# Kernel tuning notes

Measured on AMD Instinct MI355X. Metric: run time of the kernel, lower is better.

The kernel has to match this reference:

```python
import jax, jax.numpy as jnp
import numpy as np

N_NODES = 100000
N_EDGES = 3200000


def gcn_conv(x, edge_index, W, b, num_nodes):
    """PyG GCNConv: x' = D^{-1/2} (A + I) D^{-1/2} (x W) + b (symmetric norm, self-loops)."""
    x = x @ W  # [N, out]
    loop = jnp.arange(num_nodes, dtype=edge_index.dtype)
    src = jnp.concatenate([edge_index[0], loop])
    dst = jnp.concatenate([edge_index[1], loop])
    # degree over destination nodes (incl. self loops)
    deg = jax.ops.segment_sum(jnp.ones_like(dst, dtype=x.dtype), dst, num_segments=num_nodes)
    dinv = jnp.where(deg > 0, jax.lax.rsqrt(deg), 0.0)
    norm = dinv[src] * dinv[dst]  # [E + N]
    msg = x[src] * norm[:, None]  # gather + scale
    out = jax.ops.segment_sum(msg, dst, num_segments=num_nodes)  # scatter-add
    return out + b


def setup_inputs() -> dict:
    key = jax.random.key(0)
    k = jax.random.split(key, 5)
    x = jax.random.normal(k[0], (N_NODES, 256), dtype=jnp.float32)
    edge_index = jax.random.randint(k[1], (2, N_EDGES), 0, N_NODES, dtype=jnp.int64)
    W1 = jax.random.normal(k[2], (256, 16), dtype=jnp.float32) * (1.0 / np.sqrt(256))
    b1 = jnp.zeros((16,), dtype=jnp.float32)
    W2 = jax.random.normal(k[3], (16, 8), dtype=jnp.float32) * (1.0 / np.sqrt(16))
    b2 = jnp.zeros((8,), dtype=jnp.float32)
    return {"x": x, "edge_index": edge_index, "W1": W1, "b1": b1, "W2": W2, "b2": b2}


def reference(x, edge_index, W1, b1, W2, b2):
    n = x.shape[0]
    h = gcn_conv(x, edge_index, W1, b1, n)
    h = jax.nn.relu(h)
    # dropout is identity in eval mode (training=False)
    h = gcn_conv(h, edge_index, W2, b2, n)
    return jax.nn.log_softmax(h, axis=1)
```

## Files before the change

### kernel.cpp

```cpp
#include <hip/hip_runtime.h>

#define NN 100000
#define NE 3200000
#define NB 391
#define CAP 9216
#define PB 16
#define CH_A (256 * PB)
#define FXS 65536.0f
#define FXI (1.0f / 65536.0f)

typedef _Float16 half4 __attribute__((ext_vector_type(4)));
typedef _Float16 half8 __attribute__((ext_vector_type(8)));

__device__ __forceinline__ float4 f4fma(float s, float4 a, float4 c) {
  c.x = fmaf(s, a.x, c.x); c.y = fmaf(s, a.y, c.y);
  c.z = fmaf(s, a.z, c.z); c.w = fmaf(s, a.w, c.w);
  return c;
}

template<int CTRL>
__device__ __forceinline__ float4 quad_bcast(float4 v) {
  float4 r;
  r.x = __int_as_float(__builtin_amdgcn_update_dpp(__float_as_int(v.x), __float_as_int(v.x), CTRL, 0xF, 0xF, false));
  r.y = __int_as_float(__builtin_amdgcn_update_dpp(__float_as_int(v.y), __float_as_int(v.y), CTRL, 0xF, 0xF, false));
  r.z = __int_as_float(__builtin_amdgcn_update_dpp(__float_as_int(v.z), __float_as_int(v.z), CTRL, 0xF, 0xF, false));
  r.w = __int_as_float(__builtin_amdgcn_update_dpp(__float_as_int(v.w), __float_as_int(v.w), CTRL, 0xF, 0xF, false));
  return r;
}

__global__ __launch_bounds__(256) void bin_kernel(const int* __restrict__ ei,
                                                  int* __restrict__ bucket_cursor,
                                                  int* __restrict__ pairs) {
  __shared__ int  cnt[4][NB];
  __shared__ int  wcur[4][NB];
  __shared__ int  lbase[NB];
  __shared__ int  gbase[NB];
  __shared__ int  sc[512];
  __shared__ int2 stage[CH_A];
  __shared__ int  w64flag;
  int t = threadIdx.x;
  int wv = t >> 6;
  for (int k = t; k < 4 * NB; k += 256) (&cnt[0][0])[k] = 0;
  if (t < 64) {
    int o = (t < 32) ? ei[2 * t + 1] : 0;
    unsigned long long bl = __ballot(o != 0);
    if (t == 0) w64flag = (bl == 0ULL) ? 1 : 0;
  }
  __syncthreads();
  bool w64 = (w64flag != 0);
  int base = blockIdx.x * CH_A;
  int nval = min(CH_A, NE - base);
  int s[PB], d[PB];
  if (w64) {
#pragma unroll
    for (int i = 0; i < 8; ++i) {
      int e0 = base + i * 512 + 2 * t;
      if (e0 < NE) {
        int4 svv = *(const int4*)(ei + 2 * (size_t)e0);
        int4 dvv = *(const int4*)(ei + 2 * (size_t)NE + 2 * (size_t)e0);
        s[2 * i] = svv.x; s[2 * i + 1] = svv.z;
        d[2 * i] = dvv.x; d[2 * i + 1] = dvv.z;
        atomicAdd(&cnt[wv][dvv.x >> 8], 1);
        atomicAdd(&cnt[wv][dvv.z >> 8], 1);
      } else {
        d[2 * i] = -1; d[2 * i + 1] = -1;
      }
    }
  } else {
#pragma unroll
    for (int i = 0; i < PB; ++i) {
      int e = base + i * 256 + t;
      if (e < NE) {
        s[i] = ei[e];
        d[i] = ei[NE + e];
        atomicAdd(&cnt[wv][d[i] >> 8], 1);
      } else {
        d[i] = -1;
      }
    }
  }
  __syncthreads();
  int tA = (t < NB) ? cnt[0][t] + cnt[1][t] + cnt[2][t] + cnt[3][t] : 0;
  int tB = (t + 256 < NB) ? cnt[0][t + 256] + cnt[1][t + 256] + cnt[2][t + 256] + cnt[3][t + 256] : 0;
  sc[t] = tA; sc[t + 256] = tB;
  __syncthreads();
#pragma unroll
  for (int off = 1; off < 512; off <<= 1) {
    int u0 = (t >= off) ? sc[t - off] : 0;
    int u1 = (t + 256 >= off) ? sc[t + 256 - off] : 0;
    __syncthreads();
    sc[t] += u0; sc[t + 256] += u1;
    __syncthreads();
  }
#pragma unroll
  for (int h = 0; h < 2; ++h) {
    int k = t + h * 256;
    if (k < NB) {
      int tot = (h == 0) ? tA : tB;
      int lb = sc[k] - tot;
      lbase[k] = lb;
      gbase[k] = (tot > 0) ? atomicAdd(&bucket_cursor[k], tot) : 0;
      int c0 = cnt[0][k], c1 = cnt[1][k], c2 = cnt[2][k];
      wcur[0][k] = lb;
      wcur[1][k] = lb + c0;
      wcur[2][k] = lb + c0 + c1;
      wcur[3][k] = lb + c0 + c1 + c2;
    }
  }
  __syncthreads();
#pragma unroll
  for (int i = 0; i < PB; ++i) {
    if (d[i] >= 0) {
      int b = d[i] >> 8;
      int slot = atomicAdd(&wcur[wv][b], 1);
      stage[slot] = make_int2(s[i], d[i]);
    }
  }
  __syncthreads();
  for (int k = t; k < nval; k += 256) {
    int2 p = stage[k];
    int b = p.y >> 8;
    pairs[(size_t)b * CAP + gbase[b] + (k - lbase[b])] = p.x | ((p.y & 255) << 24);
  }
}

__global__ __launch_bounds__(512) void hist_kernel(const int* __restrict__ pairs,
                                                   const int* __restrict__ bucket_cursor,
                                                   float* __restrict__ dinv) {
  __shared__ int hist[2][256];
  int t = threadIdx.x;
  int b = blockIdx.x;
  int cnt_b = bucket_cursor[b];
  size_t in_base = (size_t)b * CAP;
  if (t < 256) { hist[0][t] = 0; hist[1][t] = 0; }
  __syncthreads();
  int hs = t >> 8;
  for (int i = t; i < cnt_b; i += 512) {
    int pk = pairs[in_base + i];
    atomicAdd(&hist[hs][((unsigned)pk) >> 24], 1);
  }
  __syncthreads();
  if (t < 256) {
    int n = b * 256 + t;
    if (n < NN)
      dinv[n] = rsqrtf((float)(hist[0][t] + hist[1][t]) + 1.0f);
  }
}

__global__ __launch_bounds__(256) void gemm1_kernel(const float* __restrict__ x,
                                                    const float* __restrict__ W1,
                                                    const float* __restrict__ dinv,
                                                    _Float16* __restrict__ xw1h) {
  const int lane = threadIdx.x & 63;
  const int wv   = threadIdx.x >> 6;
  const int node0 = (blockIdx.x * 4 + wv) * 8;
  const int cg = lane >> 2;
  const int jl = lane & 3;
  float4 w[16];
#pragma unroll
  for (int k = 0; k < 4; ++k)
#pragma unroll
    for (int c = 0; c < 4; ++c)
      w[k * 4 + c] = *(const float4*)(W1 + (cg * 16 + k * 4 + c) * 16 + jl * 4);
  float4 xv[8];
#pragma unroll
  for (int i = 0; i < 8; ++i)
    xv[i] = *(const float4*)(x + (size_t)(node0 + i) * 256 + lane * 4);
  float4 acc[8];
#pragma unroll
  for (int i = 0; i < 8; ++i) acc[i] = make_float4(0.f, 0.f, 0.f, 0.f);
#pragma unroll
  for (int i = 0; i < 8; ++i) {
    float4 b = quad_bcast<0x00>(xv[i]);
    acc[i] = f4fma(b.x, w[0], acc[i]);  acc[i] = f4fma(b.y, w[1], acc[i]);
    acc[i] = f4fma(b.z, w[2], acc[i]);  acc[i] = f4fma(b.w, w[3], acc[i]);
  }
#pragma unroll
  for (int i = 0; i < 8; ++i) {
    float4 b = quad_bcast<0x55>(xv[i]);
    acc[i] = f4fma(b.x, w[4], acc[i]);  acc[i] = f4fma(b.y, w[5], acc[i]);
    acc[i] = f4fma(b.z, w[6], acc[i]);  acc[i] = f4fma(b.w, w[7], acc[i]);
  }
#pragma unroll
  for (int i = 0; i < 8; ++i) {
    float4 b = quad_bcast<0xAA>(xv[i]);
    acc[i] = f4fma(b.x, w[8], acc[i]);  acc[i] = f4fma(b.y, w[9], acc[i]);
    acc[i] = f4fma(b.z, w[10], acc[i]); acc[i] = f4fma(b.w, w[11], acc[i]);
  }
#pragma unroll
  for (int i = 0; i < 8; ++i) {
    float4 b = quad_bcast<0xFF>(xv[i]);
    acc[i] = f4fma(b.x, w[12], acc[i]); acc[i] = f4fma(b.y, w[13], acc[i]);
    acc[i] = f4fma(b.z, w[14], acc[i]); acc[i] = f4fma(b.w, w[15], acc[i]);
  }
#pragma unroll
  for (int m = 4; m <= 32; m <<= 1) {
#pragma unroll
    for (int i = 0; i < 8; ++i) {
      acc[i].x += __shfl_xor(acc[i].x, m);
      acc[i].y += __shfl_xor(acc[i].y, m);
      acc[i].z += __shfl_xor(acc[i].z, m);
      acc[i].w += __shfl_xor(acc[i].w, m);
    }
  }
  if (lane < 4) {
#pragma unroll
    for (int i = 0; i < 8; ++i) {
      float dn = dinv[node0 + i];
      float4 a = acc[i];
      half4 hv;
      hv[0] = (_Float16)(a.x * dn); hv[1] = (_Float16)(a.y * dn);
      hv[2] = (_Float16)(a.z * dn); hv[3] = (_Float16)(a.w * dn);
      *(half4*)(xw1h + (size_t)(node0 + i) * 16 + lane * 4) = hv;
    }
  }
}

__global__ __launch_bounds__(1024) void agg1_kernel(const int* __restrict__ pairs,
                                                    const int* __restrict__ bucket_cursor,
                                                    const float* __restrict__ dinv,
                                                    const _Float16* __restrict__ xw1h,
                                                    const float* __restrict__ W2,
                                                    const float* __restrict__ b1,
                                                    _Float16* __restrict__ h1w2h) {
  __shared__ int acc[16][257];
  int t = threadIdx.x;
  int b = blockIdx.x;
  int cnt_b = bucket_cursor[b];
  size_t in_base = (size_t)b * CAP;
  for (int k = t; k < 16 * 257; k += 1024) (&acc[0][0])[k] = 0;
  __syncthreads();
  for (int i = t; i < cnt_b; i += 1024) {
    int pk = pairs[in_base + i];
    int s  = pk & 0xFFFFFF;
    int nl = ((unsigned)pk) >> 24;
    half8 v0 = *(const half8*)(xw1h + (size_t)s * 16);
    half8 v1 = *(const half8*)(xw1h + (size_t)s * 16 + 8);
#pragma unroll
    for (int j = 0; j < 8; ++j)
      atomicAdd(&acc[j][nl], __float2int_rn((float)v0[j] * FXS));
#pragma unroll
    for (int j = 0; j < 8; ++j)
      atomicAdd(&acc[8 + j][nl], __float2int_rn((float)v1[j] * FXS));
  }
  __syncthreads();
  int n0 = t >> 2, sub = t & 3;
  int n = b * 256 + n0;
  if (n < NN) {
    float dn = dinv[n];
    half4 sv = *(const half4*)(xw1h + (size_t)n * 16 + sub * 4);
    float4 bv = *(const float4*)(b1 + sub * 4);
    float bb[4] = {bv.x, bv.y, bv.z, bv.w};
    float p[8] = {0.f, 0.f, 0.f, 0.f, 0.f, 0.f, 0.f, 0.f};
    const float4* W2v = (const float4*)W2;
#pragma unroll
    for (int f = 0; f < 4; ++f) {
      int fg = sub * 4 + f;
      float aggv = (float)acc[fg][n0] * FXI;
      float h = fmaxf(fmaf(dn, aggv + (float)sv[f], bb[f]), 0.f);
      float4 wlo = W2v[fg * 2];
      float4 whi = W2v[fg * 2 + 1];
      p[0] = fmaf(h, wlo.x, p[0]); p[1] = fmaf(h, wlo.y, p[1]);
      p[2] = fmaf(h, wlo.z, p[2]); p[3] = fmaf(h, wlo.w, p[3]);
      p[4] = fmaf(h, whi.x, p[4]); p[5] = fmaf(h, whi.y, p[5]);
      p[6] = fmaf(h, whi.z, p[6]); p[7] = fmaf(h, whi.w, p[7]);
    }
#pragma unroll
    for (int m = 1; m <= 2; m <<= 1)
#pragma unroll
      for (int j = 0; j < 8; ++j)
        p[j] += __shfl_xor(p[j], m);
    if (sub == 0) {
      half8 hv;
#pragma unroll
      for (int j = 0; j < 8; ++j) hv[j] = (_Float16)(p[j] * dn);
      *(half8*)(h1w2h + (size_t)n * 8) = hv;
    }
  }
}

__global__ __launch_bounds__(1024) void agg2_kernel(const int* __restrict__ pairs,
                                                    const int* __restrict__ bucket_cursor,
                                                    const float* __restrict__ dinv,
                                                    const _Float16* __restrict__ h1w2h,
                                                    const float* __restrict__ b2,
                                                    float* __restrict__ out) {
  __shared__ int acc[8][257];
  int t = threadIdx.x;
  int b = blockIdx.x;
  int cnt_b = bucket_cursor[b];
  size_t in_base = (size_t)b * CAP;
  for (int k = t; k < 8 * 257; k += 1024) (&acc[0][0])[k] = 0;
  __syncthreads();
  for (int i = t; i < cnt_b; i += 1024) {
    int pk = pairs[in_base + i];
    int s  = pk & 0xFFFFFF;
    int nl = ((unsigned)pk) >> 24;
    half8 v = *(const half8*)(h1w2h + (size_t)s * 8);
#pragma unroll
    for (int j = 0; j < 8; ++j)
      atomicAdd(&acc[j][nl], __float2int_rn((float)v[j] * FXS));
  }
  __syncthreads();
  if (t < 512) {
    int n0 = t >> 1, q = t & 1;
    int n = b * 256 + n0;
    if (n < NN) {
      float dn = dinv[n];
      half4 sv = *(const half4*)(h1w2h + (size_t)n * 8 + q * 4);
      float4 bv = *(const float4*)(b2 + q * 4);
      float v0 = fmaf(dn, (float)acc[q * 4 + 0][n0] * FXI + (float)sv[0], bv.x);
      float v1 = fmaf(dn, (float)acc[q * 4 + 1][n0] * FXI + (float)sv[1], bv.y);
      float v2 = fmaf(dn, (float)acc[q * 4 + 2][n0] * FXI + (float)sv[2], bv.z);
      float v3 = fmaf(dn, (float)acc[q * 4 + 3][n0] * FXI + (float)sv[3], bv.w);
      float mh = fmaxf(fmaxf(v0, v1), fmaxf(v2, v3));
      float m = fmaxf(mh, __shfl_xor(mh, 1));
      float se = expf(v0 - m) + expf(v1 - m) + expf(v2 - m) + expf(v3 - m);
      float st = se + __shfl_xor(se, 1);
      float ls = m + logf(st);
      *(float4*)(out + (size_t)n * 8 + q * 4) = make_float4(v0 - ls, v1 - ls, v2 - ls, v3 - ls);
    }
  }
}

extern "C" void kernel_launch(void* const* d_in, const int* in_sizes, int n_in,
                              void* d_out, int out_size, void* d_ws, size_t ws_size,
                              hipStream_t stream) {
  const float* x  = (const float*)d_in[0];
  const int*   ei = (const int*)d_in[1];
  const float* W1 = (const float*)d_in[2];
  const float* b1 = (const float*)d_in[3];
  const float* W2 = (const float*)d_in[4];
  const float* b2 = (const float*)d_in[5];
  float* out = (float*)d_out;

  float*    dinv          = (float*)d_ws;
  int*      bucket_cursor = (int*)(dinv + NN);
  int*      pairs         = (int*)dinv + 100400;
  _Float16* xw1h  = (_Float16*)(pairs + (size_t)NB * CAP);
  _Float16* h1w2h = xw1h + (size_t)16 * NN;

  hipMemsetAsync(bucket_cursor, 0, (size_t)NB * sizeof(int), stream);
  bin_kernel<<<(NE + CH_A - 1) / CH_A, 256, 0, stream>>>(ei, bucket_cursor, pairs);
  hist_kernel<<<NB, 512, 0, stream>>>(pairs, bucket_cursor, dinv);
  gemm1_kernel<<<NN / 32, 256, 0, stream>>>(x, W1, dinv, xw1h);
  agg1_kernel<<<NB, 1024, 0, stream>>>(pairs, bucket_cursor, dinv, xw1h, W2, b1, h1w2h);
  agg2_kernel<<<NB, 1024, 0, stream>>>(pairs, bucket_cursor, dinv, h1w2h, b2, out);
}
```

Measured before the change: 291.5 us.

## Halve destination bucket width to 128 nodes and double bucket count

Destination buckets now cover 128 nodes instead of 256, giving 782 buckets of smaller capacity, so the aggregation and histogram kernels launch about twice as many blocks with half the threads each. The binning kernel switches to two per-half-block counters with a four-buckets-per-thread scan to fit the larger bucket count in shared memory. gemm1 now handles 4 nodes per wavefront with 8 waves per block, trading register use for more waves. The aim is better CU load balance and occupancy in the scatter phases. The cost is more global cursor atomics, scattered writes in binning, and a tighter per-bucket capacity margin.

```diff
diff --git a/kernel.cpp b/kernel.cpp
--- a/kernel.cpp
+++ b/kernel.cpp
@@ -2,8 +2,8 @@
 
 #define NN 100000
 #define NE 3200000
-#define NB 391
-#define CAP 9216
+#define NB 782
+#define CAP 4864
 #define PB 16
 #define CH_A (256 * PB)
 #define FXS 65536.0f
@@ -31,16 +31,16 @@
 __global__ __launch_bounds__(256) void bin_kernel(const int* __restrict__ ei,
                                                   int* __restrict__ bucket_cursor,
                                                   int* __restrict__ pairs) {
-  __shared__ int  cnt[4][NB];
-  __shared__ int  wcur[4][NB];
+  __shared__ int  cnt[2][NB];
+  __shared__ int  wcur[2][NB];
   __shared__ int  lbase[NB];
   __shared__ int  gbase[NB];
-  __shared__ int  sc[512];
+  __shared__ int  sc[256];
   __shared__ int2 stage[CH_A];
   __shared__ int  w64flag;
   int t = threadIdx.x;
-  int wv = t >> 6;
-  for (int k = t; k < 4 * NB; k += 256) (&cnt[0][0])[k] = 0;
+  int wp = t >> 7;
+  for (int k = t; k < 2 * NB; k += 256) (&cnt[0][0])[k] = 0;
   if (t < 64) {
     int o = (t < 32) ? ei[2 * t + 1] : 0;
     unsigned long long bl = __ballot(o != 0);
@@ -60,8 +60,8 @@
         int4 dvv = *(const int4*)(ei + 2 * (size_t)NE + 2 * (size_t)e0);
         s[2 * i] = svv.x; s[2 * i + 1] = svv.z;
         d[2 * i] = dvv.x; d[2 * i + 1] = dvv.z;
-        atomicAdd(&cnt[wv][dvv.x >> 8], 1);
-        atomicAdd(&cnt[wv][dvv.z >> 8], 1);
+        atomicAdd(&cnt[wp][dvv.x >> 7], 1);
+        atomicAdd(&cnt[wp][dvv.z >> 7], 1);
       } else {
         d[2 * i] = -1; d[2 * i + 1] = -1;
       }
@@ -73,87 +73,90 @@
       if (e < NE) {
         s[i] = ei[e];
         d[i] = ei[NE + e];
-        atomicAdd(&cnt[wv][d[i] >> 8], 1);
+        atomicAdd(&cnt[wp][d[i] >> 7], 1);
       } else {
         d[i] = -1;
       }
     }
   }
   __syncthreads();
-  int tA = (t < NB) ? cnt[0][t] + cnt[1][t] + cnt[2][t] + cnt[3][t] : 0;
-  int tB = (t + 256 < NB) ? cnt[0][t + 256] + cnt[1][t + 256] + cnt[2][t + 256] + cnt[3][t + 256] : 0;
-  sc[t] = tA; sc[t + 256] = tB;
-  __syncthreads();
-#pragma unroll
-  for (int off = 1; off < 512; off <<= 1) {
-    int u0 = (t >= off) ? sc[t - off] : 0;
-    int u1 = (t + 256 >= off) ? sc[t + 256 - off] : 0;
+  int b0 = 4 * t;
+  int c4[4];
+  int sum4 = 0;
+#pragma unroll
+  for (int j = 0; j < 4; ++j) {
+    int bb = b0 + j;
+    c4[j] = (bb < NB) ? cnt[0][bb] + cnt[1][bb] : 0;
+    sum4 += c4[j];
+  }
+  sc[t] = sum4;
+  __syncthreads();
+#pragma unroll
+  for (int off = 1; off < 256; off <<= 1) {
+    int u = (t >= off) ? sc[t - off] : 0;
     __syncthreads();
-    sc[t] += u0; sc[t + 256] += u1;
+    sc[t] += u;
     __syncthreads();
   }
-#pragma unroll
-  for (int h = 0; h < 2; ++h) {
-    int k = t + h * 256;
-    if (k < NB) {
-      int tot = (h == 0) ? tA : tB;
-      int lb = sc[k] - tot;
-      lbase[k] = lb;
-      gbase[k] = (tot > 0) ? atomicAdd(&bucket_cursor[k], tot) : 0;
-      int c0 = cnt[0][k], c1 = cnt[1][k], c2 = cnt[2][k];
-      wcur[0][k] = lb;
-      wcur[1][k] = lb + c0;
-      wcur[2][k] = lb + c0 + c1;
-      wcur[3][k] = lb + c0 + c1 + c2;
+  int run = sc[t] - sum4;
+#pragma unroll
+  for (int j = 0; j < 4; ++j) {
+    int bb = b0 + j;
+    if (bb < NB) {
+      lbase[bb] = run;
+      gbase[bb] = (c4[j] > 0) ? atomicAdd(&bucket_cursor[bb], c4[j]) : 0;
+      wcur[0][bb] = run;
+      wcur[1][bb] = run + cnt[0][bb];
+      run += c4[j];
     }
   }
   __syncthreads();
 #pragma unroll
   for (int i = 0; i < PB; ++i) {
     if (d[i] >= 0) {
-      int b = d[i] >> 8;
-      int slot = atomicAdd(&wcur[wv][b], 1);
+      int b = d[i] >> 7;
+      int slot = atomicAdd(&wcur[wp][b], 1);
       stage[slot] = make_int2(s[i], d[i]);
     }
   }
   __syncthreads();
   for (int k = t; k < nval; k += 256) {
     int2 p = stage[k];
-    int b = p.y >> 8;
-    pairs[(size_t)b * CAP + gbase[b] + (k - lbase[b])] = p.x | ((p.y & 255) << 24);
-  }
-}
-
-__global__ __launch_bounds__(512) void hist_kernel(const int* __restrict__ pairs,
+    int b = p.y >> 7;
+    pairs[(size_t)b * CAP + gbase[b] + (k - lbase[b])] = p.x | ((p.y & 127) << 24);
+  }
+}
+
+__global__ __launch_bounds__(256) void hist_kernel(const int* __restrict__ pairs,
                                                    const int* __restrict__ bucket_cursor,
                                                    float* __restrict__ dinv) {
-  __shared__ int hist[2][256];
+  __shared__ int hist[2][128];
   int t = threadIdx.x;
   int b = blockIdx.x;
   int cnt_b = bucket_cursor[b];
   size_t in_base = (size_t)b * CAP;
-  if (t < 256) { hist[0][t] = 0; hist[1][t] = 0; }
-  __syncthreads();
-  int hs = t >> 8;
-  for (int i = t; i < cnt_b; i += 512) {
+  if (t < 128) { hist[0][t] = 0; hist[1][t] = 0; }
+  __syncthreads();
+  int hs = t >> 7;
+  for (int i = t; i < cnt_b; i += 256) {
     int pk = pairs[in_base + i];
     atomicAdd(&hist[hs][((unsigned)pk) >> 24], 1);
   }
   __syncthreads();
-  if (t < 256) {
-    int n = b * 256 + t;
+  if (t < 128) {
+    int n = b * 128 + t;
     if (n < NN)
       dinv[n] = rsqrtf((float)(hist[0][t] + hist[1][t]) + 1.0f);
   }
 }
 
-__global__ __launch_bounds__(256) void gemm1_kernel(const float* __restrict__ x,
+__global__ __launch_bounds__(512) void gemm1_kernel(const float* __restrict__ x,
                                                     const float* __restrict__ W1,
                                                     const float* __restrict__ dinv,
                                                     _Float16* __restrict__ xw1h) {
   const int lane = threadIdx.x & 63;
   const int wv   = threadIdx.x >> 6;
-  const int node0 = (blockIdx.x * 4 + wv) * 8;
+  const int node0 = (blockIdx.x * 8 + wv) * 4;
   const int cg = lane >> 2;
   const int jl = lane & 3;
   float4 w[16];
@@ -162,33 +165,33 @@
 #pragma unroll
     for (int c = 0; c < 4; ++c)
       w[k * 4 + c] = *(const float4*)(W1 + (cg * 16 + k * 4 + c) * 16 + jl * 4);
-  float4 xv[8];
-#pragma unroll
-  for (int i = 0; i < 8; ++i)
+  float4 xv[4];
+#pragma unroll
+  for (int i = 0; i < 4; ++i)
     xv[i] = *(const float4*)(x + (size_t)(node0 + i) * 256 + lane * 4);
-  float4 acc[8];
-#pragma unroll
-  for (int i = 0; i < 8; ++i) acc[i] = make_float4(0.f, 0.f, 0.f, 0.f);
-#pragma unroll
-  for (int i = 0; i < 8; ++i) {
+  float4 acc[4];
+#pragma unroll
+  for (int i = 0; i < 4; ++i) acc[i] = make_float4(0.f, 0.f, 0.f, 0.f);
+#pragma unroll
+  for (int i = 0; i < 4; ++i) {
     float4 b = quad_bcast<0x00>(xv[i]);
     acc[i] = f4fma(b.x, w[0], acc[i]);  acc[i] = f4fma(b.y, w[1], acc[i]);
     acc[i] = f4fma(b.z, w[2], acc[i]);  acc[i] = f4fma(b.w, w[3], acc[i]);
   }
 #pragma unroll
-  for (int i = 0; i < 8; ++i) {
+  for (int i = 0; i < 4; ++i) {
     float4 b = quad_bcast<0x55>(xv[i]);
     acc[i] = f4fma(b.x, w[4], acc[i]);  acc[i] = f4fma(b.y, w[5], acc[i]);
     acc[i] = f4fma(b.z, w[6], acc[i]);  acc[i] = f4fma(b.w, w[7], acc[i]);
   }
 #pragma unroll
-  for (int i = 0; i < 8; ++i) {
+  for (int i = 0; i < 4; ++i) {
     float4 b = quad_bcast<0xAA>(xv[i]);
     acc[i] = f4fma(b.x, w[8], acc[i]);  acc[i] = f4fma(b.y, w[9], acc[i]);
     acc[i] = f4fma(b.z, w[10], acc[i]); acc[i] = f4fma(b.w, w[11], acc[i]);
   }
 #pragma unroll
-  for (int i = 0; i < 8; ++i) {
+  for (int i = 0; i < 4; ++i) {
     float4 b = quad_bcast<0xFF>(xv[i]);
     acc[i] = f4fma(b.x, w[12], acc[i]); acc[i] = f4fma(b.y, w[13], acc[i]);
     acc[i] = f4fma(b.z, w[14], acc[i]); acc[i] = f4fma(b.w, w[15], acc[i]);
@@ -196,7 +199,7 @@
 #pragma unroll
   for (int m = 4; m <= 32; m <<= 1) {
 #pragma unroll
-    for (int i = 0; i < 8; ++i) {
+    for (int i = 0; i < 4; ++i) {
       acc[i].x += __shfl_xor(acc[i].x, m);
       acc[i].y += __shfl_xor(acc[i].y, m);
       acc[i].z += __shfl_xor(acc[i].z, m);
@@ -205,7 +208,7 @@
   }
   if (lane < 4) {
 #pragma unroll
-    for (int i = 0; i < 8; ++i) {
+    for (int i = 0; i < 4; ++i) {
       float dn = dinv[node0 + i];
       float4 a = acc[i];
       half4 hv;
@@ -216,21 +219,21 @@
   }
 }
 
-__global__ __launch_bounds__(1024) void agg1_kernel(const int* __restrict__ pairs,
-                                                    const int* __restrict__ bucket_cursor,
-                                                    const float* __restrict__ dinv,
-                                                    const _Float16* __restrict__ xw1h,
-                                                    const float* __restrict__ W2,
-                                                    const float* __restrict__ b1,
-                                                    _Float16* __restrict__ h1w2h) {
-  __shared__ int acc[16][257];
+__global__ __launch_bounds__(512) void agg1_kernel(const int* __restrict__ pairs,
+                                                   const int* __restrict__ bucket_cursor,
+                                                   const float* __restrict__ dinv,
+                                                   const _Float16* __restrict__ xw1h,
+                                                   const float* __restrict__ W2,
+                                                   const float* __restrict__ b1,
+                                                   _Float16* __restrict__ h1w2h) {
+  __shared__ int acc[16][129];
   int t = threadIdx.x;
   int b = blockIdx.x;
   int cnt_b = bucket_cursor[b];
   size_t in_base = (size_t)b * CAP;
-  for (int k = t; k < 16 * 257; k += 1024) (&acc[0][0])[k] = 0;
-  __syncthreads();
-  for (int i = t; i < cnt_b; i += 1024) {
+  for (int k = t; k < 16 * 129; k += 512) (&acc[0][0])[k] = 0;
+  __syncthreads();
+  for (int i = t; i < cnt_b; i += 512) {
     int pk = pairs[in_base + i];
     int s  = pk & 0xFFFFFF;
     int nl = ((unsigned)pk) >> 24;
@@ -245,7 +248,7 @@
   }
   __syncthreads();
   int n0 = t >> 2, sub = t & 3;
-  int n = b * 256 + n0;
+  int n = b * 128 + n0;
   if (n < NN) {
     float dn = dinv[n];
     half4 sv = *(const half4*)(xw1h + (size_t)n * 16 + sub * 4);
@@ -279,20 +282,20 @@
   }
 }
 
-__global__ __launch_bounds__(1024) void agg2_kernel(const int* __restrict__ pairs,
-                                                    const int* __restrict__ bucket_cursor,
-                                                    const float* __restrict__ dinv,
-                                                    const _Float16* __restrict__ h1w2h,
-                                                    const float* __restrict__ b2,
-                                                    float* __restrict__ out) {
-  __shared__ int acc[8][257];
+__global__ __launch_bounds__(512) void agg2_kernel(const int* __restrict__ pairs,
+                                                   const int* __restrict__ bucket_cursor,
+                                                   const float* __restrict__ dinv,
+                                                   const _Float16* __restrict__ h1w2h,
+                                                   const float* __restrict__ b2,
+                                                   float* __restrict__ out) {
+  __shared__ int acc[8][129];
   int t = threadIdx.x;
   int b = blockIdx.x;
   int cnt_b = bucket_cursor[b];
   size_t in_base = (size_t)b * CAP;
-  for (int k = t; k < 8 * 257; k += 1024) (&acc[0][0])[k] = 0;
-  __syncthreads();
-  for (int i = t; i < cnt_b; i += 1024) {
+  for (int k = t; k < 8 * 129; k += 512) (&acc[0][0])[k] = 0;
+  __syncthreads();
+  for (int i = t; i < cnt_b; i += 512) {
     int pk = pairs[in_base + i];
     int s  = pk & 0xFFFFFF;
     int nl = ((unsigned)pk) >> 24;
@@ -302,9 +305,9 @@
       atomicAdd(&acc[j][nl], __float2int_rn((float)v[j] * FXS));
   }
   __syncthreads();
-  if (t < 512) {
+  if (t < 256) {
     int n0 = t >> 1, q = t & 1;
-    int n = b * 256 + n0;
+    int n = b * 128 + n0;
     if (n < NN) {
       float dn = dinv[n];
       half4 sv = *(const half4*)(h1w2h + (size_t)n * 8 + q * 4);
@@ -336,14 +339,14 @@
 
   float*    dinv          = (float*)d_ws;
   int*      bucket_cursor = (int*)(dinv + NN);
-  int*      pairs         = (int*)dinv + 100400;
+  int*      pairs         = (int*)dinv + 100800;
   _Float16* xw1h  = (_Float16*)(pairs + (size_t)NB * CAP);
   _Float16* h1w2h = xw1h + (size_t)16 * NN;
 
   hipMemsetAsync(bucket_cursor, 0, (size_t)NB * sizeof(int), stream);
   bin_kernel<<<(NE + CH_A - 1) / CH_A, 256, 0, stream>>>(ei, bucket_cursor, pairs);
-  hist_kernel<<<NB, 512, 0, stream>>>(pairs, bucket_cursor, dinv);
-  gemm1_kernel<<<NN / 32, 256, 0, stream>>>(x, W1, dinv, xw1h);
-  agg1_kernel<<<NB, 1024, 0, stream>>>(pairs, bucket_cursor, dinv, xw1h, W2, b1, h1w2h);
-  agg2_kernel<<<NB, 1024, 0, stream>>>(pairs, bucket_cursor, dinv, h1w2h, b2, out);
-}
+  hist_kernel<<<NB, 256, 0, stream>>>(pairs, bucket_cursor, dinv);
+  gemm1_kernel<<<NN / 32, 512, 0, stream>>>(x, W1, dinv, xw1h);
+  agg1_kernel<<<NB, 512, 0, stream>>>(pairs, bucket_cursor, dinv, xw1h, W2, b1, h1w2h);
+  agg2_kernel<<<NB, 512, 0, stream>>>(pairs, bucket_cursor, dinv, h1w2h, b2, out);
+}
```

Result: slower. 329.6 us (+13.0%).

## Merge edge binning and first GEMM into one kernel, defer source-degree scaling

Applied to the files above, without the earlier changes.

The edge-binning kernel and the x@W1 GEMM now run as disjoint block ranges of a single launch, which removes the GEMM's dependency on dinv so both memory-bound phases can overlap. Source-side dinv scaling moves from the GEMM epilogue into agg1, which gathers dinv[s] per edge, and the self-loop term is scaled by dn explicitly. The cost is an extra random 4-byte gather per edge in agg1 and larger shared-memory and register use in the combined kernel, which may lower occupancy for the GEMM blocks.

```diff
diff --git a/kernel.cpp b/kernel.cpp
--- a/kernel.cpp
+++ b/kernel.cpp
@@ -6,6 +6,8 @@
 #define CAP 9216
 #define PB 16
 #define CH_A (256 * PB)
+#define BIN_NBLK ((NE + CH_A - 1) / CH_A)
+#define GEMM_NBLK (NN / 32)
 #define FXS 65536.0f
 #define FXI (1.0f / 65536.0f)
 
@@ -28,99 +30,168 @@
   return r;
 }
 
-__global__ __launch_bounds__(256) void bin_kernel(const int* __restrict__ ei,
-                                                  int* __restrict__ bucket_cursor,
-                                                  int* __restrict__ pairs) {
-  __shared__ int  cnt[4][NB];
-  __shared__ int  wcur[4][NB];
-  __shared__ int  lbase[NB];
-  __shared__ int  gbase[NB];
-  __shared__ int  sc[512];
-  __shared__ int2 stage[CH_A];
-  __shared__ int  w64flag;
+__global__ __launch_bounds__(256) void k1_kernel(const int* __restrict__ ei,
+                                                 int* __restrict__ bucket_cursor,
+                                                 int* __restrict__ pairs,
+                                                 const float* __restrict__ x,
+                                                 const float* __restrict__ W1,
+                                                 _Float16* __restrict__ xw1h) {
   int t = threadIdx.x;
-  int wv = t >> 6;
-  for (int k = t; k < 4 * NB; k += 256) (&cnt[0][0])[k] = 0;
-  if (t < 64) {
-    int o = (t < 32) ? ei[2 * t + 1] : 0;
-    unsigned long long bl = __ballot(o != 0);
-    if (t == 0) w64flag = (bl == 0ULL) ? 1 : 0;
-  }
-  __syncthreads();
-  bool w64 = (w64flag != 0);
-  int base = blockIdx.x * CH_A;
-  int nval = min(CH_A, NE - base);
-  int s[PB], d[PB];
-  if (w64) {
+  if (blockIdx.x < BIN_NBLK) {
+    __shared__ int  cnt[4][NB];
+    __shared__ int  wcur[4][NB];
+    __shared__ int  lbase[NB];
+    __shared__ int  gbase[NB];
+    __shared__ int  sc[512];
+    __shared__ int2 stage[CH_A];
+    __shared__ int  w64flag;
+    int wv = t >> 6;
+    for (int k = t; k < 4 * NB; k += 256) (&cnt[0][0])[k] = 0;
+    if (t < 64) {
+      int o = (t < 32) ? ei[2 * t + 1] : 0;
+      unsigned long long bl = __ballot(o != 0);
+      if (t == 0) w64flag = (bl == 0ULL) ? 1 : 0;
+    }
+    __syncthreads();
+    bool w64 = (w64flag != 0);
+    int base = blockIdx.x * CH_A;
+    int nval = min(CH_A, NE - base);
+    int s[PB], d[PB];
+    if (w64) {
+#pragma unroll
+      for (int i = 0; i < 8; ++i) {
+        int e0 = base + i * 512 + 2 * t;
+        if (e0 < NE) {
+          int4 svv = *(const int4*)(ei + 2 * (size_t)e0);
+          int4 dvv = *(const int4*)(ei + 2 * (size_t)NE + 2 * (size_t)e0);
+          s[2 * i] = svv.x; s[2 * i + 1] = svv.z;
+          d[2 * i] = dvv.x; d[2 * i + 1] = dvv.z;
+          atomicAdd(&cnt[wv][dvv.x >> 8], 1);
+          atomicAdd(&cnt[wv][dvv.z >> 8], 1);
+        } else {
+          d[2 * i] = -1; d[2 * i + 1] = -1;
+        }
+      }
+    } else {
+#pragma unroll
+      for (int i = 0; i < PB; ++i) {
+        int e = base + i * 256 + t;
+        if (e < NE) {
+          s[i] = ei[e];
+          d[i] = ei[NE + e];
+          atomicAdd(&cnt[wv][d[i] >> 8], 1);
+        } else {
+          d[i] = -1;
+        }
+      }
+    }
+    __syncthreads();
+    int tA = (t < NB) ? cnt[0][t] + cnt[1][t] + cnt[2][t] + cnt[3][t] : 0;
+    int tB = (t + 256 < NB) ? cnt[0][t + 256] + cnt[1][t + 256] + cnt[2][t + 256] + cnt[3][t + 256] : 0;
+    sc[t] = tA; sc[t + 256] = tB;
+    __syncthreads();
+#pragma unroll
+    for (int off = 1; off < 512; off <<= 1) {
+      int u0 = (t >= off) ? sc[t - off] : 0;
+      int u1 = (t + 256 >= off) ? sc[t + 256 - off] : 0;
+      __syncthreads();
+      sc[t] += u0; sc[t + 256] += u1;
+      __syncthreads();
+    }
+#pragma unroll
+    for (int h = 0; h < 2; ++h) {
+      int k = t + h * 256;
+      if (k < NB) {
+        int tot = (h == 0) ? tA : tB;
+        int lb = sc[k] - tot;
+        lbase[k] = lb;
+        gbase[k] = (tot > 0) ? atomicAdd(&bucket_cursor[k], tot) : 0;
+        int c0 = cnt[0][k], c1 = cnt[1][k], c2 = cnt[2][k];
+        wcur[0][k] = lb;
+        wcur[1][k] = lb + c0;
+        wcur[2][k] = lb + c0 + c1;
+        wcur[3][k] = lb + c0 + c1 + c2;
+      }
+    }
+    __syncthreads();
+#pragma unroll
+    for (int i = 0; i < PB; ++i) {
+      if (d[i] >= 0) {
+        int b = d[i] >> 8;
+        int slot = atomicAdd(&wcur[wv][b], 1);
+        stage[slot] = make_int2(s[i], d[i]);
+      }
+    }
+    __syncthreads();
+    for (int k = t; k < nval; k += 256) {
+      int2 p = stage[k];
+      int b = p.y >> 8;
+      pairs[(size_t)b * CAP + gbase[b] + (k - lbase[b])] = p.x | ((p.y & 255) << 24);
+    }
+  } else {
+    const int bid  = blockIdx.x - BIN_NBLK;
+    const int lane = t & 63;
+    const int wv   = t >> 6;
+    const int node0 = (bid * 4 + wv) * 8;
+    const int cg = lane >> 2;
+    const int jl = lane & 3;
+    float4 w[16];
+#pragma unroll
+    for (int k = 0; k < 4; ++k)
+#pragma unroll
+      for (int c = 0; c < 4; ++c)
+        w[k * 4 + c] = *(const float4*)(W1 + (cg * 16 + k * 4 + c) * 16 + jl * 4);
+    float4 xv[8];
+#pragma unroll
+    for (int i = 0; i < 8; ++i)
+      xv[i] = *(const float4*)(x + (size_t)(node0 + i) * 256 + lane * 4);
+    float4 acc[8];
+#pragma unroll
+    for (int i = 0; i < 8; ++i) acc[i] = make_float4(0.f, 0.f, 0.f, 0.f);
 #pragma unroll
     for (int i = 0; i < 8; ++i) {
-      int e0 = base + i * 512 + 2 * t;
-      if (e0 < NE) {
-        int4 svv = *(const int4*)(ei + 2 * (size_t)e0);
-        int4 dvv = *(const int4*)(ei + 2 * (size_t)NE + 2 * (size_t)e0);
-        s[2 * i] = svv.x; s[2 * i + 1] = svv.z;
-        d[2 * i] = dvv.x; d[2 * i + 1] = dvv.z;
-        atomicAdd(&cnt[wv][dvv.x >> 8], 1);
-        atomicAdd(&cnt[wv][dvv.z >> 8], 1);
-      } else {
-        d[2 * i] = -1; d[2 * i + 1] = -1;
-      }
-    }
-  } else {
-#pragma unroll
-    for (int i = 0; i < PB; ++i) {
-      int e = base + i * 256 + t;
-      if (e < NE) {
-        s[i] = ei[e];
-        d[i] = ei[NE + e];
-        atomicAdd(&cnt[wv][d[i] >> 8], 1);
-      } else {
-        d[i] = -1;
-      }
-    }
-  }
-  __syncthreads();
-  int tA = (t < NB) ? cnt[0][t] + cnt[1][t] + cnt[2][t] + cnt[3][t] : 0;
-  int tB = (t + 256 < NB) ? cnt[0][t + 256] + cnt[1][t + 256] + cnt[2][t + 256] + cnt[3][t + 256] : 0;
-  sc[t] = tA; sc[t + 256] = tB;
-  __syncthreads();
-#pragma unroll
-  for (int off = 1; off < 512; off <<= 1) {
-    int u0 = (t >= off) ? sc[t - off] : 0;
-    int u1 = (t + 256 >= off) ? sc[t + 256 - off] : 0;
-    __syncthreads();
-    sc[t] += u0; sc[t + 256] += u1;
-    __syncthreads();
-  }
-#pragma unroll
-  for (int h = 0; h < 2; ++h) {
-    int k = t + h * 256;
-    if (k < NB) {
-      int tot = (h == 0) ? tA : tB;
-      int lb = sc[k] - tot;
-      lbase[k] = lb;
-      gbase[k] = (tot > 0) ? atomicAdd(&bucket_cursor[k], tot) : 0;
-      int c0 = cnt[0][k], c1 = cnt[1][k], c2 = cnt[2][k];
-      wcur[0][k] = lb;
-      wcur[1][k] = lb + c0;
-      wcur[2][k] = lb + c0 + c1;
-      wcur[3][k] = lb + c0 + c1 + c2;
-    }
-  }
-  __syncthreads();
-#pragma unroll
-  for (int i = 0; i < PB; ++i) {
-    if (d[i] >= 0) {
-      int b = d[i] >> 8;
-      int slot = atomicAdd(&wcur[wv][b], 1);
-      stage[slot] = make_int2(s[i], d[i]);
-    }
-  }
-  __syncthreads();
-  for (int k = t; k < nval; k += 256) {
-    int2 p = stage[k];
-    int b = p.y >> 8;
-    pairs[(size_t)b * CAP + gbase[b] + (k - lbase[b])] = p.x | ((p.y & 255) << 24);
+      float4 b = quad_bcast<0x00>(xv[i]);
+      acc[i] = f4fma(b.x, w[0], acc[i]);  acc[i] = f4fma(b.y, w[1], acc[i]);
+      acc[i] = f4fma(b.z, w[2], acc[i]);  acc[i] = f4fma(b.w, w[3], acc[i]);
+    }
+#pragma unroll
+    for (int i = 0; i < 8; ++i) {
+      float4 b = quad_bcast<0x55>(xv[i]);
+      acc[i] = f4fma(b.x, w[4], acc[i]);  acc[i] = f4fma(b.y, w[5], acc[i]);
+      acc[i] = f4fma(b.z, w[6], acc[i]);  acc[i] = f4fma(b.w, w[7], acc[i]);
+    }
+#pragma unroll
+    for (int i = 0; i < 8; ++i) {
+      float4 b = quad_bcast<0xAA>(xv[i]);
+      acc[i] = f4fma(b.x, w[8], acc[i]);  acc[i] = f4fma(b.y, w[9], acc[i]);
+      acc[i] = f4fma(b.z, w[10], acc[i]); acc[i] = f4fma(b.w, w[11], acc[i]);
+    }
+#pragma unroll
+    for (int i = 0; i < 8; ++i) {
+      float4 b = quad_bcast<0xFF>(xv[i]);
+      acc[i] = f4fma(b.x, w[12], acc[i]); acc[i] = f4fma(b.y, w[13], acc[i]);
+      acc[i] = f4fma(b.z, w[14], acc[i]); acc[i] = f4fma(b.w, w[15], acc[i]);
+    }
+#pragma unroll
+    for (int m = 4; m <= 32; m <<= 1) {
+#pragma unroll
+      for (int i = 0; i < 8; ++i) {
+        acc[i].x += __shfl_xor(acc[i].x, m);
+        acc[i].y += __shfl_xor(acc[i].y, m);
+        acc[i].z += __shfl_xor(acc[i].z, m);
+        acc[i].w += __shfl_xor(acc[i].w, m);
+      }
+    }
+    if (lane < 4) {
+#pragma unroll
+      for (int i = 0; i < 8; ++i) {
+        float4 a = acc[i];
+        half4 hv;
+        hv[0] = (_Float16)a.x; hv[1] = (_Float16)a.y;
+        hv[2] = (_Float16)a.z; hv[3] = (_Float16)a.w;
+        *(half4*)(xw1h + (size_t)(node0 + i) * 16 + lane * 4) = hv;
+      }
+    }
   }
 }
 
@@ -144,75 +215,6 @@
     int n = b * 256 + t;
     if (n < NN)
       dinv[n] = rsqrtf((float)(hist[0][t] + hist[1][t]) + 1.0f);
-  }
-}
-
-__global__ __launch_bounds__(256) void gemm1_kernel(const float* __restrict__ x,
-                                                    const float* __restrict__ W1,
-                                                    const float* __restrict__ dinv,
-                                                    _Float16* __restrict__ xw1h) {
-  const int lane = threadIdx.x & 63;
-  const int wv   = threadIdx.x >> 6;
-  const int node0 = (blockIdx.x * 4 + wv) * 8;
-  const int cg = lane >> 2;
-  const int jl = lane & 3;
-  float4 w[16];
-#pragma unroll
-  for (int k = 0; k < 4; ++k)
-#pragma unroll
-    for (int c = 0; c < 4; ++c)
-      w[k * 4 + c] = *(const float4*)(W1 + (cg * 16 + k * 4 + c) * 16 + jl * 4);
-  float4 xv[8];
-#pragma unroll
-  for (int i = 0; i < 8; ++i)
-    xv[i] = *(const float4*)(x + (size_t)(node0 + i) * 256 + lane * 4);
-  float4 acc[8];
-#pragma unroll
-  for (int i = 0; i < 8; ++i) acc[i] = make_float4(0.f, 0.f, 0.f, 0.f);
-#pragma unroll
-  for (int i = 0; i < 8; ++i) {
-    float4 b = quad_bcast<0x00>(xv[i]);
-    acc[i] = f4fma(b.x, w[0], acc[i]);  acc[i] = f4fma(b.y, w[1], acc[i]);
-    acc[i] = f4fma(b.z, w[2], acc[i]);  acc[i] = f4fma(b.w, w[3], acc[i]);
-  }
-#pragma unroll
-  for (int i = 0; i < 8; ++i) {
-    float4 b = quad_bcast<0x55>(xv[i]);
-    acc[i] = f4fma(b.x, w[4], acc[i]);  acc[i] = f4fma(b.y, w[5], acc[i]);
-    acc[i] = f4fma(b.z, w[6], acc[i]);  acc[i] = f4fma(b.w, w[7], acc[i]);
-  }
-#pragma unroll
-  for (int i = 0; i < 8; ++i) {
-    float4 b = quad_bcast<0xAA>(xv[i]);
-    acc[i] = f4fma(b.x, w[8], acc[i]);  acc[i] = f4fma(b.y, w[9], acc[i]);
-    acc[i] = f4fma(b.z, w[10], acc[i]); acc[i] = f4fma(b.w, w[11], acc[i]);
-  }
-#pragma unroll
-  for (int i = 0; i < 8; ++i) {
-    float4 b = quad_bcast<0xFF>(xv[i]);
-    acc[i] = f4fma(b.x, w[12], acc[i]); acc[i] = f4fma(b.y, w[13], acc[i]);
-    acc[i] = f4fma(b.z, w[14], acc[i]); acc[i] = f4fma(b.w, w[15], acc[i]);
-  }
-#pragma unroll
-  for (int m = 4; m <= 32; m <<= 1) {
-#pragma unroll
-    for (int i = 0; i < 8; ++i) {
-      acc[i].x += __shfl_xor(acc[i].x, m);
-      acc[i].y += __shfl_xor(acc[i].y, m);
-      acc[i].z += __shfl_xor(acc[i].z, m);
-      acc[i].w += __shfl_xor(acc[i].w, m);
-    }
-  }
-  if (lane < 4) {
-#pragma unroll
-    for (int i = 0; i < 8; ++i) {
-      float dn = dinv[node0 + i];
-      float4 a = acc[i];
-      half4 hv;
-      hv[0] = (_Float16)(a.x * dn); hv[1] = (_Float16)(a.y * dn);
-      hv[2] = (_Float16)(a.z * dn); hv[3] = (_Float16)(a.w * dn);
-      *(half4*)(xw1h + (size_t)(node0 + i) * 16 + lane * 4) = hv;
-    }
   }
 }
 
@@ -234,14 +236,15 @@
     int pk = pairs[in_base + i];
     int s  = pk & 0xFFFFFF;
     int nl = ((unsigned)pk) >> 24;
+    float dvs = dinv[s] * FXS;
     half8 v0 = *(const half8*)(xw1h + (size_t)s * 16);
     half8 v1 = *(const half8*)(xw1h + (size_t)s * 16 + 8);
 #pragma unroll
     for (int j = 0; j < 8; ++j)
-      atomicAdd(&acc[j][nl], __float2int_rn((float)v0[j] * FXS));
+      atomicAdd(&acc[j][nl], __float2int_rn((float)v0[j] * dvs));
 #pragma unroll
     for (int j = 0; j < 8; ++j)
-      atomicAdd(&acc[8 + j][nl], __float2int_rn((float)v1[j] * FXS));
+      atomicAdd(&acc[8 + j][nl], __float2int_rn((float)v1[j] * dvs));
   }
   __syncthreads();
   int n0 = t >> 2, sub = t & 3;
@@ -257,7 +260,7 @@
     for (int f = 0; f < 4; ++f) {
       int fg = sub * 4 + f;
       float aggv = (float)acc[fg][n0] * FXI;
-      float h = fmaxf(fmaf(dn, aggv + (float)sv[f], bb[f]), 0.f);
+      float h = fmaxf(fmaf(dn, aggv + dn * (float)sv[f], bb[f]), 0.f);
       float4 wlo = W2v[fg * 2];
       float4 whi = W2v[fg * 2 + 1];
       p[0] = fmaf(h, wlo.x, p[0]); p[1] = fmaf(h, wlo.y, p[1]);
@@ -341,9 +344,8 @@
   _Float16* h1w2h = xw1h + (size_t)16 * NN;
 
   hipMemsetAsync(bucket_cursor, 0, (size_t)NB * sizeof(int), stream);
-  bin_kernel<<<(NE + CH_A - 1) / CH_A, 256, 0, stream>>>(ei, bucket_cursor, pairs);
+  k1_kernel<<<BIN_NBLK + GEMM_NBLK, 256, 0, stream>>>(ei, bucket_cursor, pairs, x, W1, xw1h);
   hist_kernel<<<NB, 512, 0, stream>>>(pairs, bucket_cursor, dinv);
-  gemm1_kernel<<<NN / 32, 256, 0, stream>>>(x, W1, dinv, xw1h);
   agg1_kernel<<<NB, 1024, 0, stream>>>(pairs, bucket_cursor, dinv, xw1h, W2, b1, h1w2h);
   agg2_kernel<<<NB, 1024, 0, stream>>>(pairs, bucket_cursor, dinv, h1w2h, b2, out);
 }
```

Measured after the change: 287.6 us. About the same (-1.3%).
